# Optimization experiments

Measured on AMD Instinct MI355X. Metric: run time of the kernel, lower is better.

## Reference

```python
import jax, jax.numpy as jnp
import numpy as np

NEG = -1e9

def _leaky(x, slope):
    return jnp.where(x >= 0, x, slope * x)

def _mlp_sig(x, w1, b1, w2, b2):
    # Linear -> LeakyReLU(0.01) -> Linear -> Sigmoid  (a graph_discover expert)
    return jax.nn.sigmoid(_leaky(x @ w1 + b1, 0.01) @ w2 + b2)

def _gatv2(x, adj, wl, bl, wr, br, we, att, bias):
    # Dense-masked GATv2Conv (PyG semantics): edge s->t exists iff adj[b,s,t] != 0,
    # edge_attr is the adjacency value (edge_dim=1), heads concatenated.
    B, Np, _ = x.shape
    heads, out_ch = att.shape
    xl = (x @ wl + bl).reshape(B, Np, heads, out_ch)  # source transform (messages)
    xr = (x @ wr + br).reshape(B, Np, heads, out_ch)  # target transform
    adjT = jnp.swapaxes(adj, 1, 2)                    # [b, target, source]
    ea = adjT[..., None, None] * we.reshape(heads, out_ch)   # lin_edge (no bias)
    e = _leaky(xl[:, None, :, :, :] + xr[:, :, None, :, :] + ea, 0.2)  # (B,T,S,H,O)
    logits = jnp.einsum('btsho,ho->btsh', e, att)
    m = adjT != 0
    logits = jnp.where(m[..., None], logits, NEG)
    alpha = jax.nn.softmax(logits, axis=2) * m[..., None]    # zero rows with no in-edges
    out = jnp.einsum('btsh,bsho->btho', alpha, xl)
    return out.reshape(B, Np, heads * out_ch) + bias

def _forward(latent, gumbel_noise,
             d0_w1, d0_b1, d0_w2, d0_b2,
             d1_w1, d1_b1, d1_w2, d1_b2,
             a_w, a_b,
             g1_wl, g1_bl, g1_wr, g1_br, g1_we, g1_att, g1_bias,
             g2_wl, g2_bl, g2_wr, g2_br, g2_we, g2_att, g2_bias):
    B, C, Hh, Ww = latent.shape
    N = Hh * Ww
    lat = jnp.transpose(latent, (0, 2, 3, 1)).reshape(B, N, C)
    # positional encoding (dropout = identity in eval)
    pos = jnp.arange(N, dtype=jnp.float32)[:, None]
    div = jnp.exp(jnp.arange(0, C, 2, dtype=jnp.float32) * (-np.log(10000.0) / C))
    pe = jnp.zeros((N, C), lat.dtype).at[:, 0::2].set(jnp.sin(pos * div)).at[:, 1::2].set(jnp.cos(pos * div))
    pl = lat + pe
    mask = jnp.zeros((B, N, 1), lat.dtype)  # forward() hardcodes mask = 0

    # pairwise node concat: inp[b, i*N+j] = [pl[b,i], pl[b,j]]
    ni = jnp.repeat(pl, N, axis=1)
    nj = jnp.tile(pl, (1, N, 1))
    inp = jnp.concatenate([ni, nj], axis=-1)  # (B, N*N, 2C)
    no_inter = _mlp_sig(inp, d0_w1, d0_b1, d0_w2, d0_b2).reshape(B, N, N)
    # action = zeros -> argmax = 0 for every row -> all rows routed to expert graph_discovers[1]
    inter = _mlp_sig(inp, d1_w1, d1_b1, d1_w2, d1_b2).reshape(B, N, N)
    adj = no_inter * (1 - mask) + inter * mask

    # differentiable Bernoulli via hard gumbel-softmax (straight-through)
    logits = jnp.log(jnp.clip(jnp.stack([1 - adj, adj], axis=-1), 1e-4))
    y = jax.nn.softmax(logits + gumbel_noise, axis=-1)
    y_hard = jax.nn.one_hot(jnp.argmax(y, axis=-1), 2, dtype=y.dtype)
    cg = (y_hard + y - jax.lax.stop_gradient(y))[..., 1]
    weighted = adj * cg

    # _compute_y, noise='off': append action node, pad adjacency (right col = 1, bottom row = 0)
    action = jnp.zeros((B, a_w.shape[0]), lat.dtype)
    action_node = action @ a_w + a_b
    nodes = jnp.concatenate([pl, action_node[:, None, :]], axis=1)  # (B, N+1, C)
    adj_p = jnp.pad(weighted, ((0, 0), (0, 0), (0, 1)), constant_values=1.0)
    adj_p = jnp.pad(adj_p, ((0, 0), (0, 1), (0, 0)), constant_values=0.0)

    x1 = _leaky(_gatv2(nodes, adj_p, g1_wl, g1_bl, g1_wr, g1_br, g1_we, g1_att, g1_bias), 0.01)
    x2 = _gatv2(x1, adj_p, g2_wl, g2_bl, g2_wr, g2_br, g2_we, g2_att, g2_bias)  # (B, N+1, heads*C)
    ny = x2[:, :N, :]
    # action argmax = 0 -> gathered head is columns [C, 2C)
    out = ny[..., :C] * (1 - mask) + ny[..., C:2 * C] * mask
    return jax.nn.softmax(out, axis=-1)

def setup_inputs() -> dict:
    key = jax.random.key(0)
    ks = jax.random.split(key, 32)
    B, C, Hh, Ww = 4, 64, 14, 14
    N = Hh * Ww
    A = 4
    heads = 1 + A
    D0, O1 = 800, 100
    f32 = jnp.float32
    def nrm(k, shp, sc=0.05):
        return jax.random.normal(k, shp, f32) * sc
    return {
        'latent': jax.random.normal(ks[0], (B, C, Hh, Ww), f32),
        'gumbel_noise': jax.random.gumbel(ks[1], (B, N, N, 2), f32),
        'd0_w1': nrm(ks[2], (2 * C, D0)), 'd0_b1': jnp.zeros((D0,), f32),
        'd0_w2': nrm(ks[3], (D0, 1)), 'd0_b2': jnp.zeros((1,), f32),
        'd1_w1': nrm(ks[4], (2 * C, D0)), 'd1_b1': jnp.zeros((D0,), f32),
        'd1_w2': nrm(ks[5], (D0, 1)), 'd1_b2': jnp.zeros((1,), f32),
        'a_w': nrm(ks[6], (A, C)), 'a_b': nrm(ks[7], (C,)),
        'g1_wl': nrm(ks[8], (C, heads * O1)), 'g1_bl': jnp.zeros((heads * O1,), f32),
        'g1_wr': nrm(ks[9], (C, heads * O1)), 'g1_br': jnp.zeros((heads * O1,), f32),
        'g1_we': nrm(ks[10], (heads * O1,)), 'g1_att': nrm(ks[11], (heads, O1)),
        'g1_bias': jnp.zeros((heads * O1,), f32),
        'g2_wl': nrm(ks[12], (heads * O1, heads * C)), 'g2_bl': jnp.zeros((heads * C,), f32),
        'g2_wr': nrm(ks[13], (heads * O1, heads * C)), 'g2_br': jnp.zeros((heads * C,), f32),
        'g2_we': nrm(ks[14], (heads * C,)), 'g2_att': nrm(ks[15], (heads, C)),
        'g2_bias': jnp.zeros((heads * C,), f32),
    }

def reference(latent, gumbel_noise,
              d0_w1, d0_b1, d0_w2, d0_b2,
              d1_w1, d1_b1, d1_w2, d1_b2,
              a_w, a_b,
              g1_wl, g1_bl, g1_wr, g1_br, g1_we, g1_att, g1_bias,
              g2_wl, g2_bl, g2_wr, g2_br, g2_we, g2_att, g2_bias):
    return _forward(latent, gumbel_noise,
                    d0_w1, d0_b1, d0_w2, d0_b2,
                    d1_w1, d1_b1, d1_w2, d1_b2,
                    a_w, a_b,
                    g1_wl, g1_bl, g1_wr, g1_br, g1_we, g1_att, g1_bias,
                    g2_wl, g2_bl, g2_wr, g2_br, g2_we, g2_att, g2_bias)
```

## Files before the change

kernel.cpp:

```cpp
#include <hip/hip_runtime.h>
#include <math.h>

#define NB 4
#define NN 196
#define NC 64
#define ND0 800
#define NH 5
#define NO1 100
#define NC1 500
#define NO2 64
#define TT 2
#define JC 4
#define JW 200
#define TQ 2
#define RT 7
#define RW 2
#define NEGF -1000000000.0f
#define TH_MARGIN 0.002f

__global__ void __launch_bounds__(256)
k_head(const float* __restrict__ latent,
       const float* __restrict__ w1, const float* __restrict__ b1,
       const float* __restrict__ wl, const float* __restrict__ bl,
       const float* __restrict__ wr, const float* __restrict__ br,
       double* __restrict__ U_d, double* __restrict__ V_d,
       float* __restrict__ U_f, float* __restrict__ VT_f,
       float* __restrict__ xl1, float* __restrict__ xl1T, float* __restrict__ xr1,
       int* __restrict__ bcount) {
    __shared__ double rowd[RT][NC];
    __shared__ float  rowf[RW][NC];
    int bi = blockIdx.x;
    int tid = threadIdx.x;
    if (bi == 0 && tid == 0) *bcount = 0;
    const int NUV = NB*(NN/RT)*4;
    if (bi < NUV) {
        int b = bi / ((NN/RT)*4);
        int rem = bi % ((NN/RT)*4);
        int tile = rem >> 2;
        int q = rem & 3;
        int n0 = tile * RT;
        for (int idx = tid; idx < RT*NC; idx += 256) {
            int r = idx >> 6, c = idx & 63;
            int n = n0 + r;
            double div = exp((double)(2*(c >> 1)) * (-log(10000.0) / (double)NC));
            double ang = (double)n * div;
            double pe = (c & 1) ? cos(ang) : sin(ang);
            rowd[r][c] = (double)latent[(b*NC + c)*NN + n] + pe;
        }
        __syncthreads();
        int j = q*200 + tid;
        if (tid < 200) {
            double au[RT], av[RT];
            double bb = (double)b1[j];
            #pragma unroll
            for (int r = 0; r < RT; ++r) { au[r] = 0.0; av[r] = bb; }
            #pragma unroll 4
            for (int k = 0; k < NC; ++k) {
                double wu = (double)w1[k*ND0 + j];
                double wv = (double)w1[(NC + k)*ND0 + j];
                #pragma unroll
                for (int r = 0; r < RT; ++r) {
                    au[r] += rowd[r][k] * wu;
                    av[r] += rowd[r][k] * wv;
                }
            }
            size_t bn0 = (size_t)(b*NN + n0);
            #pragma unroll
            for (int r = 0; r < RT; ++r) {
                U_d[(bn0 + r)*ND0 + j] = au[r];
                V_d[(bn0 + r)*ND0 + j] = av[r];
                U_f[(bn0 + r)*ND0 + j] = (float)au[r];
                VT_f[((size_t)b*ND0 + j)*NN + n0 + r] = (float)av[r];
            }
        }
    } else {
        int bn2 = bi - NUV;
        int b = bn2 / (NN/RW);
        int n0 = (bn2 % (NN/RW)) * RW;
        for (int idx = tid; idx < RW*NC; idx += 256) {
            int r = idx >> 6, c = idx & 63;
            int n = n0 + r;
            double div = exp((double)(2*(c >> 1)) * (-log(10000.0) / (double)NC));
            double ang = (double)n * div;
            double pe = (c & 1) ? cos(ang) : sin(ang);
            rowf[r][c] = (float)((double)latent[(b*NC + c)*NN + n] + pe);
        }
        __syncthreads();
        for (int c = tid; c < NC1; c += 256) {
            float al0 = bl[c], ar0 = br[c];
            float al1 = al0, ar1 = ar0;
            #pragma unroll 8
            for (int k = 0; k < NC; ++k) {
                float wlk = wl[k*NC1 + c];
                float wrk = wr[k*NC1 + c];
                float p0 = rowf[0][k], p1 = rowf[1][k];
                al0 += p0 * wlk; al1 += p1 * wlk;
                ar0 += p0 * wrk; ar1 += p1 * wrk;
            }
            size_t bn0 = (size_t)(b*NN + n0);
            xl1[bn0*NC1 + c] = al0;
            xl1[(bn0 + 1)*NC1 + c] = al1;
            xr1[bn0*NC1 + c] = ar0;
            xr1[(bn0 + 1)*NC1 + c] = ar1;
            xl1T[((size_t)b*NC1 + c)*256 + n0] = al0;
            xl1T[((size_t)b*NC1 + c)*256 + n0 + 1] = al1;
        }
    }
}

__global__ void __launch_bounds__(1024)
k_adj32(const float* __restrict__ U_f, const float* __restrict__ VT,
        const float* __restrict__ w2, const float* __restrict__ b2,
        const float* __restrict__ gum, float* __restrict__ WT,
        int* __restrict__ blist, int* __restrict__ bcount) {
    __shared__ float Ul[TT][ND0];
    __shared__ float w2l[ND0];
    __shared__ float part[JC][TT][256];
    int bi = blockIdx.x;
    int b = bi / (NN/TT);
    int t0 = (bi % (NN/TT)) * TT;
    int tid = threadIdx.x;
    int s = tid & 255;
    int chunk = tid >> 8;
    for (int idx = tid; idx < TT*ND0; idx += 1024) {
        int tt = idx / ND0, j = idx - tt*ND0;
        Ul[tt][j] = U_f[((size_t)(b*NN + t0 + tt))*ND0 + j];
    }
    for (int j = tid; j < ND0; j += 1024) w2l[j] = w2[j];
    __syncthreads();
    float a0 = 0.0f, a1 = 0.0f;
    if (s < NN) {
        const float* vp = VT + ((size_t)b*ND0 + chunk*JW)*NN + s;
        int j0 = chunk*JW;
        #pragma unroll 4
        for (int jj = 0; jj < JW; ++jj) {
            float v = vp[(size_t)jj*NN];
            float w = w2l[j0 + jj];
            float h0 = Ul[0][j0 + jj] + v; h0 = (h0 >= 0.0f) ? h0 : 0.01f*h0; a0 = fmaf(h0, w, a0);
            float h1 = Ul[1][j0 + jj] + v; h1 = (h1 >= 0.0f) ? h1 : 0.01f*h1; a1 = fmaf(h1, w, a1);
        }
    }
    part[chunk][0][s] = a0;
    part[chunk][1][s] = a1;
    __syncthreads();
    if (tid < TT*NN) {
        int tt = tid / NN, ss = tid - tt*NN;
        float acc = b2[0] + part[0][tt][ss] + part[1][tt][ss]
                  + part[2][tt][ss] + part[3][tt][ss];
        int t = t0 + tt;
        float adj = 1.0f/(1.0f + expf(-acc));
        float l1 = logf(fmaxf(adj, 1e-4f));
        float l0 = logf(fmaxf(1.0f - adj, 1e-4f));
        float g0 = gum[((size_t)(b*NN + t)*NN + ss)*2 + 0];
        float g1 = gum[((size_t)(b*NN + t)*NN + ss)*2 + 1];
        float margin = (l1 + g1) - (l0 + g0);
        if (fabsf(margin) <= TH_MARGIN) {
            int li = atomicAdd(bcount, 1);
            blist[li] = (b*NN + t)*NN + ss;
        }
        WT[((size_t)(b*NN + ss))*NN + t] = (margin > 0.0f) ? adj : 0.0f;
    }
}

__global__ void __launch_bounds__(256)
k_adjfix(const double* __restrict__ U, const double* __restrict__ V,
         const float* __restrict__ w2, const float* __restrict__ b2,
         const float* __restrict__ gum, const int* __restrict__ blist,
         const int* __restrict__ bcount, float* __restrict__ WT) {
    int nfix = *bcount;
    int gwid = (blockIdx.x * blockDim.x + threadIdx.x) >> 6;
    int lane = threadIdx.x & 63;
    int nw = (gridDim.x * blockDim.x) >> 6;
    for (int i = gwid; i < nfix; i += nw) {
        int code = blist[i];
        int s = code % NN;
        int t = (code / NN) % NN;
        int b = code / (NN*NN);
        const double* up = U + ((size_t)(b*NN + t))*ND0;
        const double* vp = V + ((size_t)(b*NN + s))*ND0;
        double a = 0.0;
        for (int j = lane; j < ND0; j += 64) {
            double h = up[j] + vp[j];
            h = (h >= 0.0) ? h : 0.01*h;
            a += h * (double)w2[j];
        }
        for (int off = 32; off >= 1; off >>= 1) a += __shfl_xor(a, off);
        if (lane == 0) {
            double acc = a + (double)b2[0];
            double adj = 1.0/(1.0 + exp(-acc));
            double l1 = log(fmax(adj, 1e-4));
            double l0 = log(fmax(1.0 - adj, 1e-4));
            double g0 = (double)gum[((size_t)(b*NN + t)*NN + s)*2 + 0];
            double g1 = (double)gum[((size_t)(b*NN + t)*NN + s)*2 + 1];
            double z0 = l0 + g0, z1 = l1 + g1;
            double m = fmax(z0, z1);
            double e0 = exp(z0 - m), e1 = exp(z1 - m);
            double sm = e0 + e1;
            int cg = (e1/sm) > (e0/sm);
            WT[((size_t)(b*NN + s))*NN + t] = cg ? (float)adj : 0.0f;
        }
    }
}

__global__ void __launch_bounds__(256)
k_gat1a(const float* __restrict__ xl1T, const float* __restrict__ xr1,
        const float* __restrict__ WT, const float* __restrict__ we,
        const float* __restrict__ att, float* __restrict__ alphaG) {
    __shared__ float wred[4];
    __shared__ float mxs, sms;
    int blk = blockIdx.x;
    int t = blk % NN;
    int bh = blk / NN;
    int h = bh % NH;
    int b = bh / NH;
    int s = threadIdx.x;
    int lane = s & 63, wid = s >> 6;
    float wt = (s < NN) ? WT[((size_t)(b*NN + t))*NN + s] : 0.0f;
    const float* xT  = xl1T + ((size_t)b*NC1 + h*NO1)*256;
    const float* xr  = xr1 + ((size_t)(b*NN + t))*NC1 + h*NO1;
    const float* weh = we + h*NO1;
    const float* ath = att + h*NO1;
    float a = 0.0f;
    #pragma unroll 5
    for (int o = 0; o < NO1; ++o) {
        float x = xT[(size_t)o*256 + s];
        float v = fmaf(wt, weh[o], x + xr[o]);
        float av = ath[o];
        a += fmaxf(v, 0.0f)*av + fminf(v, 0.0f)*(0.2f*av);
    }
    bool on = (s < NN) && (wt != 0.0f);
    float m = on ? a : NEGF;
    #pragma unroll
    for (int off = 32; off >= 1; off >>= 1) m = fmaxf(m, __shfl_xor(m, off));
    if (lane == 0) wred[wid] = m;
    __syncthreads();
    if (s == 0) mxs = fmaxf(fmaxf(wred[0], wred[1]), fmaxf(wred[2], wred[3]));
    __syncthreads();
    float e = on ? expf(a - mxs) : 0.0f;
    float r = e;
    #pragma unroll
    for (int off = 32; off >= 1; off >>= 1) r += __shfl_xor(r, off);
    if (lane == 0) wred[wid] = r;
    __syncthreads();
    if (s == 0) sms = wred[0] + wred[1] + wred[2] + wred[3];
    __syncthreads();
    alphaG[(size_t)blk*256 + s] = (sms > 0.0f) ? e / sms : 0.0f;
}

__global__ void __launch_bounds__(640)
k_gat1b(const float* __restrict__ xl1, const float* __restrict__ alphaG,
        const float* __restrict__ bias, float* __restrict__ x1) {
    int blk = blockIdx.x;
    int b = blk / (NN/TQ), tq = blk % (NN/TQ);
    int tid = threadIdx.x;
    int w = tid >> 6, l = tid & 63;
    int h = w >> 1, csub = w & 1;
    int o = csub*64 + l;
    bool active = (o < NO1);
    int c = h*NO1 + (active ? o : 0);
    const float* ap = alphaG + (((size_t)b*NH + h)*NN + tq*TQ)*256;
    const float* xp = xl1 + (size_t)b*NN*NC1 + c;
    float a0 = 0.f, a1 = 0.f;
    for (int s = 0; s < NN; ++s) {
        float x = xp[(size_t)s*NC1];
        a0 = fmaf(ap[s], x, a0);
        a1 = fmaf(ap[256 + s], x, a1);
    }
    if (active) {
        float bs = bias[c];
        float v;
        v = a0 + bs; x1[((size_t)(b*NN + tq*TQ + 0))*NC1 + c] = (v >= 0.f) ? v : 0.01f*v;
        v = a1 + bs; x1[((size_t)(b*NN + tq*TQ + 1))*NC1 + c] = (v >= 0.f) ? v : 0.01f*v;
    }
}

__global__ void k_proj2(const float* __restrict__ x1, const float* __restrict__ wl, const float* __restrict__ bl,
                        const float* __restrict__ wr, const float* __restrict__ br,
                        float* __restrict__ xl2, float* __restrict__ xl2T, float* __restrict__ xr2) {
    __shared__ float row[NC1];
    __shared__ float part[256];
    int bn = blockIdx.x;
    int b = bn / NN, n = bn % NN;
    int tid = threadIdx.x;
    for (int c = tid; c < NC1; c += 256) row[c] = x1[(size_t)bn*NC1 + c];
    __syncthreads();
    int which = tid >> 7;
    int o = tid & 63;
    int half = (tid >> 6) & 1;
    const float* w = which ? wr : wl;
    float acc = 0.0f;
    for (int k = half*250; k < half*250 + 250; ++k)
        acc += row[k] * w[(size_t)k*320 + o];
    part[tid] = acc;
    __syncthreads();
    if ((tid & 64) == 0) {
        float tot = part[tid] + part[tid + 64];
        if (which == 0) {
            float v = tot + bl[o];
            xl2[(size_t)bn*NO2 + o] = v;
            xl2T[((size_t)b*NO2 + o)*256 + n] = v;
        } else {
            xr2[(size_t)bn*NO2 + o] = tot + br[o];
        }
    }
}

__global__ void __launch_bounds__(256)
k_gat2(const float* __restrict__ xl2T, const float* __restrict__ xl2,
       const float* __restrict__ xr2, const float* __restrict__ WT,
       const float* __restrict__ we, const float* __restrict__ att,
       const float* __restrict__ bias, float* __restrict__ out) {
    __shared__ float red[256], alpha_l[256], part[4][NO2];
    __shared__ float mxs, sms;
    int blk = blockIdx.x;
    int b = blk / NN, t = blk % NN;
    int s = threadIdx.x;
    float wt = (s < NN) ? WT[((size_t)(b*NN + t))*NN + s] : 0.0f;
    const float* xT = xl2T + (size_t)b*NO2*256;
    const float* xr = xr2 + ((size_t)(b*NN + t))*NO2;
    float acc = 0.0f;
    for (int c = 0; c < NO2; ++c) {
        float x = xT[(size_t)c*256 + s];
        float v = fmaf(wt, we[c], x + xr[c]);
        float av = att[c];
        acc += fmaxf(v, 0.0f)*av + fminf(v, 0.0f)*(0.2f*av);
    }
    bool on = (s < NN) && (wt != 0.0f);
    float lgt = on ? acc : NEGF;
    red[s] = lgt;
    __syncthreads();
    for (int d = 128; d >= 1; d >>= 1) {
        if (s < d) red[s] = fmaxf(red[s], red[s + d]);
        __syncthreads();
    }
    if (s == 0) mxs = red[0];
    __syncthreads();
    float e = on ? expf(acc - mxs) : 0.0f;
    red[s] = e;
    __syncthreads();
    for (int d = 128; d >= 1; d >>= 1) {
        if (s < d) red[s] += red[s + d];
        __syncthreads();
    }
    if (s == 0) sms = red[0];
    __syncthreads();
    alpha_l[s] = (sms > 0.0f) ? e / sms : 0.0f;
    __syncthreads();
    int c = s & 63, sq = s >> 6;
    float pa = 0.0f;
    const float* xp = xl2 + (size_t)b*NN*NO2 + c;
    for (int ss = sq*49; ss < sq*49 + 49; ++ss)
        pa = fmaf(alpha_l[ss], xp[(size_t)ss*NO2], pa);
    part[sq][c] = pa;
    __syncthreads();
    if (s < NO2) {
        float ny = part[0][s] + part[1][s] + part[2][s] + part[3][s] + bias[s];
        float m = ny;
        for (int off = 32; off >= 1; off >>= 1) m = fmaxf(m, __shfl_xor(m, off));
        float ee = expf(ny - m);
        float ssum = ee;
        for (int off = 32; off >= 1; off >>= 1) ssum += __shfl_xor(ssum, off);
        out[((size_t)(b*NN + t))*NO2 + s] = ee / ssum;
    }
}

extern "C" void kernel_launch(void* const* d_in, const int* in_sizes, int n_in,
                              void* d_out, int out_size, void* d_ws, size_t ws_size,
                              hipStream_t stream) {
    const float* latent  = (const float*)d_in[0];
    const float* gum     = (const float*)d_in[1];
    const float* d0_w1   = (const float*)d_in[2];
    const float* d0_b1   = (const float*)d_in[3];
    const float* d0_w2   = (const float*)d_in[4];
    const float* d0_b2   = (const float*)d_in[5];
    const float* g1_wl   = (const float*)d_in[12];
    const float* g1_bl   = (const float*)d_in[13];
    const float* g1_wr   = (const float*)d_in[14];
    const float* g1_br   = (const float*)d_in[15];
    const float* g1_we   = (const float*)d_in[16];
    const float* g1_att  = (const float*)d_in[17];
    const float* g1_bias = (const float*)d_in[18];
    const float* g2_wl   = (const float*)d_in[19];
    const float* g2_bl   = (const float*)d_in[20];
    const float* g2_wr   = (const float*)d_in[21];
    const float* g2_br   = (const float*)d_in[22];
    const float* g2_we   = (const float*)d_in[23];
    const float* g2_att  = (const float*)d_in[24];
    const float* g2_bias = (const float*)d_in[25];
    float* out = (float*)d_out;

    char* ws = (char*)d_ws;
    size_t off = 0;
    auto alloc = [&](size_t bytes) { char* p = ws + off; off += (bytes + 255) & ~(size_t)255; return (void*)p; };
    double* U_d   = (double*)alloc((size_t)NB*NN*ND0*8);
    double* V_d   = (double*)alloc((size_t)NB*NN*ND0*8);
    float*  U_f   = (float*) alloc((size_t)NB*NN*ND0*4);
    float*  VT_f  = (float*) alloc((size_t)NB*ND0*NN*4);
    float*  WT    = (float*) alloc((size_t)NB*NN*NN*4);
    float*  xl1   = (float*) alloc((size_t)NB*NN*NC1*4);
    float*  xl1T  = (float*) alloc((size_t)NB*NC1*256*4);
    float*  xr1   = (float*) alloc((size_t)NB*NN*NC1*4);
    float*  alphaG= (float*) alloc((size_t)NB*NH*NN*256*4);
    float*  x1    = (float*) alloc((size_t)NB*NN*NC1*4);
    float*  xl2   = (float*) alloc((size_t)NB*NN*NO2*4);
    float*  xl2T  = (float*) alloc((size_t)NB*NO2*256*4);
    float*  xr2   = (float*) alloc((size_t)NB*NN*NO2*4);
    int*    blist = (int*)   alloc((size_t)NB*NN*NN*4);
    int*    bcount= (int*)   alloc(256);

    hipLaunchKernelGGL(k_head,   dim3(NB*(NN/RT)*4 + NB*(NN/RW)), dim3(256), 0, stream,
                       latent, d0_w1, d0_b1, g1_wl, g1_bl, g1_wr, g1_br,
                       U_d, V_d, U_f, VT_f, xl1, xl1T, xr1, bcount);
    hipLaunchKernelGGL(k_adj32,  dim3(NB*(NN/TT)),  dim3(1024), 0, stream, U_f, VT_f, d0_w2, d0_b2, gum, WT, blist, bcount);
    hipLaunchKernelGGL(k_adjfix, dim3(256),         dim3(256),  0, stream, U_d, V_d, d0_w2, d0_b2, gum, blist, bcount, WT);
    hipLaunchKernelGGL(k_gat1a,  dim3(NB*NH*NN),    dim3(256),  0, stream, xl1T, xr1, WT, g1_we, g1_att, alphaG);
    hipLaunchKernelGGL(k_gat1b,  dim3(NB*(NN/TQ)),  dim3(640),  0, stream, xl1, alphaG, g1_bias, x1);
    hipLaunchKernelGGL(k_proj2,  dim3(NB*NN),       dim3(256),  0, stream, x1, g2_wl, g2_bl, g2_wr, g2_br, xl2, xl2T, xr2);
    hipLaunchKernelGGL(k_gat2,   dim3(NB*NN),       dim3(256),  0, stream, xl2T, xl2, xr2, WT, g2_we, g2_att, g2_bias, out);
}
```

Before: 146.4 us.

## Fuse GAT1 aggregation with layer-2 projection and process two targets per gat1a block

Merges k_gat1b and k_proj2 into one kernel. The layer-1 aggregated rows for two targets stay in shared memory and are projected by wl2/wr2 right away, which drops the x1 global round trip and one launch. k_gat1a now handles two target nodes per block, so each loaded xl1T value and attention weight is reused across both targets and the grid is halved. The trade-offs are fewer, larger blocks and more register pressure from the doubled accumulators.

```diff
diff --git a/kernel.cpp b/kernel.cpp
--- a/kernel.cpp
+++ b/kernel.cpp
@@ -12,7 +12,6 @@
 #define TT 2
 #define JC 4
 #define JW 200
-#define TQ 2
 #define RT 7
 #define RW 2
 #define NEGF -1000000000.0f
@@ -206,59 +205,82 @@
 k_gat1a(const float* __restrict__ xl1T, const float* __restrict__ xr1,
         const float* __restrict__ WT, const float* __restrict__ we,
         const float* __restrict__ att, float* __restrict__ alphaG) {
-    __shared__ float wred[4];
-    __shared__ float mxs, sms;
+    __shared__ float wred[4][2];
+    __shared__ float mxs[2], sms[2];
     int blk = blockIdx.x;
-    int t = blk % NN;
-    int bh = blk / NN;
+    int tp = blk % (NN/2);
+    int bh = blk / (NN/2);
     int h = bh % NH;
     int b = bh / NH;
+    int t0 = tp*2;
     int s = threadIdx.x;
     int lane = s & 63, wid = s >> 6;
-    float wt = (s < NN) ? WT[((size_t)(b*NN + t))*NN + s] : 0.0f;
+    float wt0 = (s < NN) ? WT[((size_t)(b*NN + t0))*NN + s] : 0.0f;
+    float wt1 = (s < NN) ? WT[((size_t)(b*NN + t0 + 1))*NN + s] : 0.0f;
     const float* xT  = xl1T + ((size_t)b*NC1 + h*NO1)*256;
-    const float* xr  = xr1 + ((size_t)(b*NN + t))*NC1 + h*NO1;
+    const float* xr0 = xr1 + ((size_t)(b*NN + t0))*NC1 + h*NO1;
+    const float* xr1p= xr1 + ((size_t)(b*NN + t0 + 1))*NC1 + h*NO1;
     const float* weh = we + h*NO1;
     const float* ath = att + h*NO1;
-    float a = 0.0f;
+    float a0 = 0.0f, a1 = 0.0f;
     #pragma unroll 5
     for (int o = 0; o < NO1; ++o) {
         float x = xT[(size_t)o*256 + s];
-        float v = fmaf(wt, weh[o], x + xr[o]);
+        float w = weh[o];
         float av = ath[o];
-        a += fmaxf(v, 0.0f)*av + fminf(v, 0.0f)*(0.2f*av);
-    }
-    bool on = (s < NN) && (wt != 0.0f);
-    float m = on ? a : NEGF;
+        float av2 = 0.2f*av;
+        float v0 = fmaf(wt0, w, x + xr0[o]);
+        float v1 = fmaf(wt1, w, x + xr1p[o]);
+        a0 += fmaxf(v0, 0.0f)*av + fminf(v0, 0.0f)*av2;
+        a1 += fmaxf(v1, 0.0f)*av + fminf(v1, 0.0f)*av2;
+    }
+    bool on0 = (s < NN) && (wt0 != 0.0f);
+    bool on1 = (s < NN) && (wt1 != 0.0f);
+    float m0 = on0 ? a0 : NEGF;
+    float m1 = on1 ? a1 : NEGF;
     #pragma unroll
-    for (int off = 32; off >= 1; off >>= 1) m = fmaxf(m, __shfl_xor(m, off));
-    if (lane == 0) wred[wid] = m;
-    __syncthreads();
-    if (s == 0) mxs = fmaxf(fmaxf(wred[0], wred[1]), fmaxf(wred[2], wred[3]));
-    __syncthreads();
-    float e = on ? expf(a - mxs) : 0.0f;
-    float r = e;
+    for (int off = 32; off >= 1; off >>= 1) {
+        m0 = fmaxf(m0, __shfl_xor(m0, off));
+        m1 = fmaxf(m1, __shfl_xor(m1, off));
+    }
+    if (lane == 0) { wred[wid][0] = m0; wred[wid][1] = m1; }
+    __syncthreads();
+    if (s < 2) mxs[s] = fmaxf(fmaxf(wred[0][s], wred[1][s]), fmaxf(wred[2][s], wred[3][s]));
+    __syncthreads();
+    float e0 = on0 ? expf(a0 - mxs[0]) : 0.0f;
+    float e1 = on1 ? expf(a1 - mxs[1]) : 0.0f;
+    float r0 = e0, r1 = e1;
     #pragma unroll
-    for (int off = 32; off >= 1; off >>= 1) r += __shfl_xor(r, off);
-    if (lane == 0) wred[wid] = r;
-    __syncthreads();
-    if (s == 0) sms = wred[0] + wred[1] + wred[2] + wred[3];
-    __syncthreads();
-    alphaG[(size_t)blk*256 + s] = (sms > 0.0f) ? e / sms : 0.0f;
+    for (int off = 32; off >= 1; off >>= 1) {
+        r0 += __shfl_xor(r0, off);
+        r1 += __shfl_xor(r1, off);
+    }
+    if (lane == 0) { wred[wid][0] = r0; wred[wid][1] = r1; }
+    __syncthreads();
+    if (s < 2) sms[s] = wred[0][s] + wred[1][s] + wred[2][s] + wred[3][s];
+    __syncthreads();
+    alphaG[((size_t)bh*NN + t0)*256 + s]     = (sms[0] > 0.0f) ? e0 / sms[0] : 0.0f;
+    alphaG[((size_t)bh*NN + t0 + 1)*256 + s] = (sms[1] > 0.0f) ? e1 / sms[1] : 0.0f;
 }
 
 __global__ void __launch_bounds__(640)
-k_gat1b(const float* __restrict__ xl1, const float* __restrict__ alphaG,
-        const float* __restrict__ bias, float* __restrict__ x1) {
+k_gat1bp(const float* __restrict__ xl1, const float* __restrict__ alphaG,
+         const float* __restrict__ bias,
+         const float* __restrict__ wl2, const float* __restrict__ bl2,
+         const float* __restrict__ wr2, const float* __restrict__ br2,
+         float* __restrict__ xl2, float* __restrict__ xl2T, float* __restrict__ xr2) {
+    __shared__ float row[2][NC1 + 4];
+    __shared__ float part[2][2][5][NO2];
     int blk = blockIdx.x;
-    int b = blk / (NN/TQ), tq = blk % (NN/TQ);
+    int b = blk / (NN/2), tp = blk % (NN/2);
+    int t0 = tp*2;
     int tid = threadIdx.x;
     int w = tid >> 6, l = tid & 63;
     int h = w >> 1, csub = w & 1;
     int o = csub*64 + l;
     bool active = (o < NO1);
     int c = h*NO1 + (active ? o : 0);
-    const float* ap = alphaG + (((size_t)b*NH + h)*NN + tq*TQ)*256;
+    const float* ap = alphaG + (((size_t)b*NH + h)*NN + t0)*256;
     const float* xp = xl1 + (size_t)b*NN*NC1 + c;
     float a0 = 0.f, a1 = 0.f;
     for (int s = 0; s < NN; ++s) {
@@ -268,39 +290,38 @@
     }
     if (active) {
         float bs = bias[c];
-        float v;
-        v = a0 + bs; x1[((size_t)(b*NN + tq*TQ + 0))*NC1 + c] = (v >= 0.f) ? v : 0.01f*v;
-        v = a1 + bs; x1[((size_t)(b*NN + tq*TQ + 1))*NC1 + c] = (v >= 0.f) ? v : 0.01f*v;
-    }
-}
-
-__global__ void k_proj2(const float* __restrict__ x1, const float* __restrict__ wl, const float* __restrict__ bl,
-                        const float* __restrict__ wr, const float* __restrict__ br,
-                        float* __restrict__ xl2, float* __restrict__ xl2T, float* __restrict__ xr2) {
-    __shared__ float row[NC1];
-    __shared__ float part[256];
-    int bn = blockIdx.x;
-    int b = bn / NN, n = bn % NN;
-    int tid = threadIdx.x;
-    for (int c = tid; c < NC1; c += 256) row[c] = x1[(size_t)bn*NC1 + c];
-    __syncthreads();
-    int which = tid >> 7;
-    int o = tid & 63;
-    int half = (tid >> 6) & 1;
-    const float* w = which ? wr : wl;
-    float acc = 0.0f;
-    for (int k = half*250; k < half*250 + 250; ++k)
-        acc += row[k] * w[(size_t)k*320 + o];
-    part[tid] = acc;
-    __syncthreads();
-    if ((tid & 64) == 0) {
-        float tot = part[tid] + part[tid + 64];
-        if (which == 0) {
-            float v = tot + bl[o];
-            xl2[(size_t)bn*NO2 + o] = v;
-            xl2T[((size_t)b*NO2 + o)*256 + n] = v;
+        float v0 = a0 + bs; row[0][c] = (v0 >= 0.f) ? v0 : 0.01f*v0;
+        float v1 = a1 + bs; row[1][c] = (v1 >= 0.f) ? v1 : 0.01f*v1;
+    }
+    __syncthreads();
+    int which = tid / 320;
+    int t5 = tid - which*320;
+    int seg = t5 >> 6;
+    int oo = t5 & 63;
+    const float* wmat = which ? wr2 : wl2;
+    float p0 = 0.f, p1 = 0.f;
+    for (int k = seg*100; k < seg*100 + 100; ++k) {
+        float wv = wmat[(size_t)k*320 + oo];
+        p0 = fmaf(row[0][k], wv, p0);
+        p1 = fmaf(row[1][k], wv, p1);
+    }
+    part[0][which][seg][oo] = p0;
+    part[1][which][seg][oo] = p1;
+    __syncthreads();
+    if (tid < 256) {
+        int r = tid >> 7;
+        int wh = (tid >> 6) & 1;
+        int o2 = tid & 63;
+        float tot = part[r][wh][0][o2] + part[r][wh][1][o2] + part[r][wh][2][o2]
+                  + part[r][wh][3][o2] + part[r][wh][4][o2];
+        int n = t0 + r;
+        size_t bn = (size_t)(b*NN + n);
+        if (wh == 0) {
+            float vv = tot + bl2[o2];
+            xl2[bn*NO2 + o2] = vv;
+            xl2T[((size_t)b*NO2 + o2)*256 + n] = vv;
         } else {
-            xr2[(size_t)bn*NO2 + o] = tot + br[o];
+            xr2[bn*NO2 + o2] = tot + br2[o2];
         }
     }
 }
@@ -401,7 +422,6 @@
     float*  xl1T  = (float*) alloc((size_t)NB*NC1*256*4);
     float*  xr1   = (float*) alloc((size_t)NB*NN*NC1*4);
     float*  alphaG= (float*) alloc((size_t)NB*NH*NN*256*4);
-    float*  x1    = (float*) alloc((size_t)NB*NN*NC1*4);
     float*  xl2   = (float*) alloc((size_t)NB*NN*NO2*4);
     float*  xl2T  = (float*) alloc((size_t)NB*NO2*256*4);
     float*  xr2   = (float*) alloc((size_t)NB*NN*NO2*4);
@@ -411,10 +431,10 @@
     hipLaunchKernelGGL(k_head,   dim3(NB*(NN/RT)*4 + NB*(NN/RW)), dim3(256), 0, stream,
                        latent, d0_w1, d0_b1, g1_wl, g1_bl, g1_wr, g1_br,
                        U_d, V_d, U_f, VT_f, xl1, xl1T, xr1, bcount);
-    hipLaunchKernelGGL(k_adj32,  dim3(NB*(NN/TT)),  dim3(1024), 0, stream, U_f, VT_f, d0_w2, d0_b2, gum, WT, blist, bcount);
-    hipLaunchKernelGGL(k_adjfix, dim3(256),         dim3(256),  0, stream, U_d, V_d, d0_w2, d0_b2, gum, blist, bcount, WT);
-    hipLaunchKernelGGL(k_gat1a,  dim3(NB*NH*NN),    dim3(256),  0, stream, xl1T, xr1, WT, g1_we, g1_att, alphaG);
-    hipLaunchKernelGGL(k_gat1b,  dim3(NB*(NN/TQ)),  dim3(640),  0, stream, xl1, alphaG, g1_bias, x1);
-    hipLaunchKernelGGL(k_proj2,  dim3(NB*NN),       dim3(256),  0, stream, x1, g2_wl, g2_bl, g2_wr, g2_br, xl2, xl2T, xr2);
-    hipLaunchKernelGGL(k_gat2,   dim3(NB*NN),       dim3(256),  0, stream, xl2T, xl2, xr2, WT, g2_we, g2_att, g2_bias, out);
-}
+    hipLaunchKernelGGL(k_adj32,  dim3(NB*(NN/TT)),     dim3(1024), 0, stream, U_f, VT_f, d0_w2, d0_b2, gum, WT, blist, bcount);
+    hipLaunchKernelGGL(k_adjfix, dim3(256),            dim3(256),  0, stream, U_d, V_d, d0_w2, d0_b2, gum, blist, bcount, WT);
+    hipLaunchKernelGGL(k_gat1a,  dim3(NB*NH*(NN/2)),   dim3(256),  0, stream, xl1T, xr1, WT, g1_we, g1_att, alphaG);
+    hipLaunchKernelGGL(k_gat1bp, dim3(NB*(NN/2)),      dim3(640),  0, stream, xl1, alphaG, g1_bias,
+                       g2_wl, g2_bl, g2_wr, g2_br, xl2, xl2T, xr2);
+    hipLaunchKernelGGL(k_gat2,   dim3(NB*NN),          dim3(256),  0, stream, xl2T, xl2, xr2, WT, g2_we, g2_att, g2_bias, out);
+}
```

Result: faster. 132.9 us (-9.2%).
